# Kernel optimization log

Measured on AMD Instinct MI355X. Metric: run time of the kernel, lower is better.

The kernel has to match this reference:

```python
import jax, jax.numpy as jnp
import numpy as np

NUM_GRIDS = 16
IN_X, IN_Z, OUT, BATCH = 32, 32, 64, 512


def _borders_cdf_grid(n_chunks):
    def inv_cdf(u):
        return np.log(2.0 * u) if u <= 0.5 else -np.log(2.0 * (1.0 - u))
    cs = 1.0 / n_chunks
    b = [inv_cdf(i * cs) for i in range(1, n_chunks)]
    left = b[0] - (b[1] - b[0])
    right = b[-1] + (b[-1] - b[-2])
    return np.array([left] + b + [right], dtype=np.float32)


def _laplace_cdf(v):
    e = jnp.exp(-jnp.abs(v))
    return jnp.where(v > 0, 1.0 - 0.5 * e, 0.5 * e)


def setup_inputs() -> dict:
    key = jax.random.key(0)
    k1, k2, k3 = jax.random.split(key, 3)
    scale = 0.1 / np.sqrt(IN_X * IN_Z)
    borders_np = _borders_cdf_grid(NUM_GRIDS)
    inv_len_np = (1.0 / (borders_np[1:] - borders_np[:-1])).astype(np.float32)
    return {
        "x": jax.random.normal(k1, (IN_X, BATCH), dtype=jnp.float32),
        "z": jax.random.normal(k2, (IN_Z, BATCH), dtype=jnp.float32),
        "func_parameter": jax.random.uniform(
            k3, (NUM_GRIDS + 1, NUM_GRIDS + 1, OUT, IN_X, IN_Z),
            dtype=jnp.float32, minval=-scale, maxval=scale),
        "borders": jnp.asarray(borders_np),
        "inverse_chunk_lengths": jnp.asarray(inv_len_np[:NUM_GRIDS]),
    }


def reference(x, z, func_parameter, borders, inverse_chunk_lengths):
    G = inverse_chunk_lengths.shape[0]
    Ix, B = x.shape
    Iz = z.shape[0]

    # data-dependent bin indices per (input_dim, batch) element
    idx_x = jnp.clip((_laplace_cdf(x) * G).astype(jnp.int32), 0, G - 1)  # [Ix,B]
    idx_z = jnp.clip((_laplace_cdf(z) * G).astype(jnp.int32), 0, G - 1)  # [Iz,B]
    dx = (x - borders[idx_x]) * inverse_chunk_lengths[idx_x]             # [Ix,B]
    dz = (z - borders[idx_z]) * inverse_chunk_lengths[idx_z]             # [Iz,B]
    idx_xn = jnp.clip(idx_x + 1, 0, G)
    idx_zn = jnp.clip(idx_z + 1, 0, G)

    # [Ix, Iz, G+1, G+1, O] so the per-(ix,iz) tables are leading-indexed
    Pt = jnp.transpose(func_parameter, (3, 4, 0, 1, 2))
    ax = jnp.arange(Ix)[:, None, None]   # [Ix,1,1]
    az = jnp.arange(Iz)[None, :, None]   # [1,Iz,1]

    def corner(ii, jj):  # ii:[Ix,1,B] or broadcastable, jj:[1,Iz,B]
        return Pt[ax, az, ii, jj]        # -> [Ix,Iz,B,O]

    ixb, ixnb = idx_x[:, None, :], idx_xn[:, None, :]
    izb, iznb = idx_z[None, :, :], idx_zn[None, :, :]
    wx, wz = dx[:, None, :], dz[None, :, :]             # [Ix,1,B],[1,Iz,B]

    out = (
        jnp.einsum('xzb,xzbo->ob', (1 - wx) * (1 - wz), corner(ixb, izb))
        + jnp.einsum('xzb,xzbo->ob', (1 - wx) * wz, corner(ixb, iznb))
        + jnp.einsum('xzb,xzbo->ob', wx * (1 - wz), corner(ixnb, izb))
        + jnp.einsum('xzb,xzbo->ob', wx * wz, corner(ixnb, iznb))
    )
    return out  # [output_dim, batch]
```

## Files before the change

kernel.cpp:

```cpp
#include <hip/hip_runtime.h>
#include <hip/hip_fp16.h>


#define NG        16
#define NB        17
#define IN_X      32
#define IN_Z      32
#define OUT_DIM   64
#define BATCH     512
#define CELLS     (NB * NB)
#define CSTRIDE   133
#define ILSTRIDE  33
#define XSTR_A    (NB * CSTRIDE)
#define STASKS    (CELLS * 32)

typedef __fp16 h2v __attribute__((ext_vector_type(2)));

__device__ __forceinline__ void grid_coord(float v,
                                           const float* __restrict__ borders,
                                           const float* __restrict__ inv_len,
                                           int& idx, float& w) {
    float e   = expf(-fabsf(v));
    float cdf = (v > 0.f) ? (1.f - 0.5f * e) : (0.5f * e);
    int t = (int)(cdf * 16.f);
    t = t < 0 ? 0 : (t > NG - 1 ? NG - 1 : t);
    idx = t;
    w = (v - borders[t]) * inv_len[t];
}

__device__ __forceinline__ unsigned pack_h2(float a, float b) {
    h2v v = __builtin_amdgcn_cvt_pkrtz(a, b);
    return __builtin_bit_cast(unsigned, v);
}
__device__ __forceinline__ __half2 u2h(unsigned u) {
    return __builtin_bit_cast(__half2, u);
}

__global__ void precompute_kernel(const float* __restrict__ x,
                                  const float* __restrict__ z,
                                  const float* __restrict__ borders,
                                  const float* __restrict__ inv_len,
                                  uint2* __restrict__ xc,
                                  uint2* __restrict__ zc,
                                  float* __restrict__ out) {
    const int gid = blockIdx.x * blockDim.x + threadIdx.x;
    out[gid] = 0.f;
    int idx; float w;
    if (gid < IN_X * BATCH) {
        grid_coord(x[gid], borders, inv_len, idx, w);
        xc[gid] = make_uint2(pack_h2(w, w), (unsigned)(idx * XSTR_A));
    } else {
        const int g = gid - IN_X * BATCH;
        grid_coord(z[g], borders, inv_len, idx, w);
        zc[g] = make_uint2(pack_h2(w, w), (unsigned)(idx * CSTRIDE));
    }
}

__global__ __launch_bounds__(1024, 1)
void bf2d_kernel(const uint2* __restrict__ xc,
                 const uint2* __restrict__ zc,
                 const float* __restrict__ P,
                 float* __restrict__ out) {
    __shared__ unsigned lds[CELLS * CSTRIDE];

    const int tid = threadIdx.x;
    const int op  = blockIdx.x & 31;
    const int iq  = blockIdx.x >> 5;
    const int o0  = op * 2;

    const float* Pb = P + (size_t)o0 * 1024 + iq * 128;
    #pragma unroll
    for (int it = 0; it < 10; ++it) {
        const int k = tid + it * 1024;
        if (k < STASKS) {
            const int c  = k >> 5;
            const int f4 = k & 31;
            const float* g = Pb + (size_t)c * 65536 + f4 * 4;
            const float4 a = *(const float4*)g;
            const float4 b = *(const float4*)(g + 1024);
            unsigned* d = &lds[c * CSTRIDE + (f4 >> 3) * ILSTRIDE
                               + ((f4 & 7) << 2)];
            d[0] = pack_h2(a.x, b.x);
            d[1] = pack_h2(a.y, b.y);
            d[2] = pack_h2(a.z, b.z);
            d[3] = pack_h2(a.w, b.w);
        }
    }
    __syncthreads();

    const int b  = tid & (BATCH - 1);
    const int ih = tid >> 9;
    const int il0 = 2 * ih, il1 = 2 * ih + 1;

    const uint2 x0 = xc[(iq * 4 + il0) * BATCH + b];
    const uint2 x1 = xc[(iq * 4 + il1) * BATCH + b];
    const __half2 wx0 = u2h(x0.x), wx1 = u2h(x1.x);
    const int xo0 = (int)x0.y + il0 * ILSTRIDE;
    const int xo1 = (int)x1.y + il1 * ILSTRIDE;

    const uint2* zp = zc + b;
    __half2 acc0 = __float2half2_rn(0.f);
    __half2 acc1 = __float2half2_rn(0.f);
    #pragma unroll 4
    for (int j = 0; j < IN_Z; ++j) {
        const uint2 zv = zp[j * BATCH];
        const __half2 wz = u2h(zv.x);
        const int     zo = (int)zv.y + j;
        {
            const int base = xo0 + zo;
            const __half2 q0 = u2h(lds[base]);
            const __half2 q1 = u2h(lds[base + CSTRIDE]);
            const __half2 v0 = u2h(lds[base + XSTR_A]);
            const __half2 v1 = u2h(lds[base + XSTR_A + CSTRIDE]);
            const __half2 zlo = __hfma2(wz, __hsub2(q1, q0), q0);
            const __half2 zhi = __hfma2(wz, __hsub2(v1, v0), v0);
            acc0 = __hadd2(acc0, __hfma2(wx0, __hsub2(zhi, zlo), zlo));
        }
        {
            const int base = xo1 + zo;
            const __half2 q0 = u2h(lds[base]);
            const __half2 q1 = u2h(lds[base + CSTRIDE]);
            const __half2 v0 = u2h(lds[base + XSTR_A]);
            const __half2 v1 = u2h(lds[base + XSTR_A + CSTRIDE]);
            const __half2 zlo = __hfma2(wz, __hsub2(q1, q0), q0);
            const __half2 zhi = __hfma2(wz, __hsub2(v1, v0), v0);
            acc1 = __hadd2(acc1, __hfma2(wx1, __hsub2(zhi, zlo), zlo));
        }
    }

    const float accx = __low2float(acc0)  + __low2float(acc1);
    const float accy = __high2float(acc0) + __high2float(acc1);

    atomicAdd(&out[o0 * BATCH + b],       accx);
    atomicAdd(&out[(o0 + 1) * BATCH + b], accy);
}

extern "C" void kernel_launch(void* const* d_in, const int* in_sizes, int n_in,
                              void* d_out, int out_size, void* d_ws, size_t ws_size,
                              hipStream_t stream) {
    const float* x       = (const float*)d_in[0];
    const float* z       = (const float*)d_in[1];
    const float* P       = (const float*)d_in[2];
    const float* borders = (const float*)d_in[3];
    const float* inv_len = (const float*)d_in[4];
    float* out = (float*)d_out;

    uint2* xc = (uint2*)d_ws;
    uint2* zc = xc + IN_X * BATCH;

    precompute_kernel<<<dim3(128), dim3(256), 0, stream>>>(
        x, z, borders, inv_len, xc, zc, out);

    bf2d_kernel<<<dim3(32 * 8), dim3(1024), 0, stream>>>(xc, zc, P, out);
}
```

Measured before the change: 125.3 us.

## Fuse coordinate precompute into main kernel and overlap with parameter loads

Removes the separate precompute kernel. Each thread now computes the Laplace-CDF bin index and weight for its x and z values inline, keeping the z coordinates packed in a 32-entry register table, and the output is zeroed with a memset. The first parameter tile load is issued before this coordinate math so the global-load latency overlaps with the ALU work. This drops one launch and the workspace round trip, but every block redundantly recomputes z coordinates for all 32 rows, and the larger register table with a fully unrolled loop raises register pressure.

```diff
diff --git a/kernel.cpp b/kernel.cpp
--- a/kernel.cpp
+++ b/kernel.cpp
@@ -16,6 +16,14 @@
 
 typedef __fp16 h2v __attribute__((ext_vector_type(2)));
 
+__device__ __forceinline__ unsigned pack_h2(float a, float b) {
+    h2v v = __builtin_amdgcn_cvt_pkrtz(a, b);
+    return __builtin_bit_cast(unsigned, v);
+}
+__device__ __forceinline__ __half2 u2h(unsigned u) {
+    return __builtin_bit_cast(__half2, u);
+}
+
 __device__ __forceinline__ void grid_coord(float v,
                                            const float* __restrict__ borders,
                                            const float* __restrict__ inv_len,
@@ -28,84 +36,85 @@
     w = (v - borders[t]) * inv_len[t];
 }
 
-__device__ __forceinline__ unsigned pack_h2(float a, float b) {
-    h2v v = __builtin_amdgcn_cvt_pkrtz(a, b);
-    return __builtin_bit_cast(unsigned, v);
-}
-__device__ __forceinline__ __half2 u2h(unsigned u) {
-    return __builtin_bit_cast(__half2, u);
-}
-
-__global__ void precompute_kernel(const float* __restrict__ x,
-                                  const float* __restrict__ z,
-                                  const float* __restrict__ borders,
-                                  const float* __restrict__ inv_len,
-                                  uint2* __restrict__ xc,
-                                  uint2* __restrict__ zc,
-                                  float* __restrict__ out) {
-    const int gid = blockIdx.x * blockDim.x + threadIdx.x;
-    out[gid] = 0.f;
-    int idx; float w;
-    if (gid < IN_X * BATCH) {
-        grid_coord(x[gid], borders, inv_len, idx, w);
-        xc[gid] = make_uint2(pack_h2(w, w), (unsigned)(idx * XSTR_A));
-    } else {
-        const int g = gid - IN_X * BATCH;
-        grid_coord(z[g], borders, inv_len, idx, w);
-        zc[g] = make_uint2(pack_h2(w, w), (unsigned)(idx * CSTRIDE));
-    }
-}
-
 __global__ __launch_bounds__(1024, 1)
-void bf2d_kernel(const uint2* __restrict__ xc,
-                 const uint2* __restrict__ zc,
-                 const float* __restrict__ P,
-                 float* __restrict__ out) {
+void bf2d_fused(const float* __restrict__ x,
+                const float* __restrict__ z,
+                const float* __restrict__ borders,
+                const float* __restrict__ inv_len,
+                const float* __restrict__ P,
+                float* __restrict__ out) {
     __shared__ unsigned lds[CELLS * CSTRIDE];
 
     const int tid = threadIdx.x;
     const int op  = blockIdx.x & 31;
     const int iq  = blockIdx.x >> 5;
     const int o0  = op * 2;
+    const int b   = tid & (BATCH - 1);
+    const int ih  = tid >> 9;
+    const int il0 = 2 * ih, il1 = 2 * ih + 1;
 
     const float* Pb = P + (size_t)o0 * 1024 + iq * 128;
+
+    float4 a0v, b0v;
+    {
+        const int c = tid >> 5, f4 = tid & 31;
+        const float* g = Pb + (size_t)c * 65536 + f4 * 4;
+        a0v = *(const float4*)g;
+        b0v = *(const float4*)(g + 1024);
+    }
+
+    unsigned ztab[IN_Z];
     #pragma unroll
-    for (int it = 0; it < 10; ++it) {
+    for (int j = 0; j < IN_Z; ++j) {
+        int idx; float w;
+        grid_coord(z[j * BATCH + b], borders, inv_len, idx, w);
+        ztab[j] = ((unsigned)(idx * CSTRIDE) << 16)
+                | (pack_h2(w, 0.f) & 0xFFFFu);
+    }
+    int xi0, xi1; float xw0f, xw1f;
+    grid_coord(x[(iq * 4 + il0) * BATCH + b], borders, inv_len, xi0, xw0f);
+    grid_coord(x[(iq * 4 + il1) * BATCH + b], borders, inv_len, xi1, xw1f);
+    const __half2 wx0 = u2h(pack_h2(xw0f, xw0f));
+    const __half2 wx1 = u2h(pack_h2(xw1f, xw1f));
+    const int xo0 = xi0 * XSTR_A + il0 * ILSTRIDE;
+    const int xo1 = xi1 * XSTR_A + il1 * ILSTRIDE;
+
+    {
+        const int c = tid >> 5, f4 = tid & 31;
+        unsigned* d = &lds[c * CSTRIDE + (f4 >> 3) * ILSTRIDE
+                           + ((f4 & 7) << 2)];
+        d[0] = pack_h2(a0v.x, b0v.x);
+        d[1] = pack_h2(a0v.y, b0v.y);
+        d[2] = pack_h2(a0v.z, b0v.z);
+        d[3] = pack_h2(a0v.w, b0v.w);
+    }
+    #pragma unroll
+    for (int it = 1; it < 10; ++it) {
         const int k = tid + it * 1024;
         if (k < STASKS) {
             const int c  = k >> 5;
             const int f4 = k & 31;
             const float* g = Pb + (size_t)c * 65536 + f4 * 4;
             const float4 a = *(const float4*)g;
-            const float4 b = *(const float4*)(g + 1024);
+            const float4 bb = *(const float4*)(g + 1024);
             unsigned* d = &lds[c * CSTRIDE + (f4 >> 3) * ILSTRIDE
                                + ((f4 & 7) << 2)];
-            d[0] = pack_h2(a.x, b.x);
-            d[1] = pack_h2(a.y, b.y);
-            d[2] = pack_h2(a.z, b.z);
-            d[3] = pack_h2(a.w, b.w);
+            d[0] = pack_h2(a.x, bb.x);
+            d[1] = pack_h2(a.y, bb.y);
+            d[2] = pack_h2(a.z, bb.z);
+            d[3] = pack_h2(a.w, bb.w);
         }
     }
     __syncthreads();
 
-    const int b  = tid & (BATCH - 1);
-    const int ih = tid >> 9;
-    const int il0 = 2 * ih, il1 = 2 * ih + 1;
-
-    const uint2 x0 = xc[(iq * 4 + il0) * BATCH + b];
-    const uint2 x1 = xc[(iq * 4 + il1) * BATCH + b];
-    const __half2 wx0 = u2h(x0.x), wx1 = u2h(x1.x);
-    const int xo0 = (int)x0.y + il0 * ILSTRIDE;
-    const int xo1 = (int)x1.y + il1 * ILSTRIDE;
-
-    const uint2* zp = zc + b;
     __half2 acc0 = __float2half2_rn(0.f);
     __half2 acc1 = __float2half2_rn(0.f);
-    #pragma unroll 4
+    #pragma unroll
     for (int j = 0; j < IN_Z; ++j) {
-        const uint2 zv = zp[j * BATCH];
-        const __half2 wz = u2h(zv.x);
-        const int     zo = (int)zv.y + j;
+        const unsigned u  = ztab[j];
+        const unsigned lo = u & 0xFFFFu;
+        const __half2 wz  = u2h(lo | (lo << 16));
+        const int     zo  = (int)(u >> 16) + j;
         {
             const int base = xo0 + zo;
             const __half2 q0 = u2h(lds[base]);
@@ -145,11 +154,7 @@
     const float* inv_len = (const float*)d_in[4];
     float* out = (float*)d_out;
 
-    uint2* xc = (uint2*)d_ws;
-    uint2* zc = xc + IN_X * BATCH;
-
-    precompute_kernel<<<dim3(128), dim3(256), 0, stream>>>(
-        x, z, borders, inv_len, xc, zc, out);
-
-    bf2d_kernel<<<dim3(32 * 8), dim3(1024), 0, stream>>>(xc, zc, P, out);
+    hipMemsetAsync(out, 0, OUT_DIM * BATCH * sizeof(float), stream);
+    bf2d_fused<<<dim3(32 * 8), dim3(1024), 0, stream>>>(
+        x, z, borders, inv_len, P, out);
 }
```

New measurement: 142.6 us. 13.7% more time.
